# Kernel tuning notes

Hardware: AMD Instinct MI355X
Metric: run time of the kernel (lower is better)

Reference implementation:

```python
import jax, jax.numpy as jnp
import numpy as np
import math

DIM = 1024
THETA = 10000.0


def rope_cos_sin(seq_len, dim, dtype=jnp.float32):
    # freqs over pairs: 1/theta^(2i/dim), angles = t * freq
    inv = 1.0 / (THETA ** (jnp.arange(0, dim, 2, dtype=jnp.float32) / dim))  # [dim/2]
    t = jnp.arange(seq_len, dtype=jnp.float32)
    ang = jnp.outer(t, inv)  # [S, dim/2]
    return jnp.cos(ang).astype(dtype), jnp.sin(ang).astype(dtype)


def apply_rotary(x, cos, sin):
    # x: [B, S, D]; treat consecutive pairs as complex (xr + i*xi)
    B, S, D = x.shape
    xr = x[..., 0::2]  # [B, S, D/2]
    xi = x[..., 1::2]
    or_ = xr * cos - xi * sin
    oi_ = xr * sin + xi * cos
    # interleave back: (..., D/2, 2) -> (..., D)
    return jnp.stack([or_, oi_], axis=-1).reshape(B, S, D)


def setup_inputs() -> dict:
    key = jax.random.key(0)
    ks = jax.random.split(key, 5)
    B, S, D = 4, 2048, DIM
    x = jax.random.normal(ks[0], (B, S, D), dtype=jnp.float32)
    s = 1.0 / math.sqrt(D)
    wq = jax.random.normal(ks[1], (D, D), dtype=jnp.float32) * s
    wk = jax.random.normal(ks[2], (D, D), dtype=jnp.float32) * s
    wv = jax.random.normal(ks[3], (D, D), dtype=jnp.float32) * s
    wo = jax.random.normal(ks[4], (D, D), dtype=jnp.float32) * s
    return {"x": x, "wq": wq, "wk": wk, "wv": wv, "wo": wo}


def reference(x, wq, wk, wv, wo):
    B, S, D = x.shape
    xq = jnp.einsum('bsd,ed->bse', x, wq)  # Linear: x @ W^T
    xk = jnp.einsum('bsd,ed->bse', x, wk)
    xv = jnp.einsum('bsd,ed->bse', x, wv)
    cos, sin = rope_cos_sin(S, D, x.dtype)
    xq = apply_rotary(xq, cos, sin)
    xk = apply_rotary(xk, cos, sin)
    scores = jnp.einsum('bqd,bkd->bqk', xq, xk) / jnp.sqrt(jnp.asarray(D, x.dtype))
    attn = jax.nn.softmax(scores, axis=-1)  # no causal mask in original
    out = jnp.einsum('bqk,bkd->bqd', attn, xv)
    return jnp.einsum('bsd,ed->bse', out, wo)
```

## Files before the change

### kernel.cpp

```cpp
#include <hip/hip_runtime.h>
#include <math.h>

typedef __attribute__((ext_vector_type(8))) short short8;
typedef __attribute__((ext_vector_type(4))) float f32x4;
typedef unsigned short u16;

__device__ __forceinline__ float b2f(u16 u) {
    union { unsigned u; float f; } c; c.u = ((unsigned)u) << 16; return c.f;
}
__device__ __forceinline__ u16 f2b(float f) {
    unsigned u = __float_as_uint(f);
    u += 0x7fffu + ((u >> 16) & 1u);
    return (u16)(u >> 16);
}

__device__ __forceinline__ void gl_lds16(const u16* g, u16* l) {
    __builtin_amdgcn_global_load_lds(
        (const __attribute__((address_space(1))) void*)g,
        (__attribute__((address_space(3))) void*)l,
        16, 0, 0);
}

__device__ __forceinline__ void xcd_swz(int& bx, int& by) {
    const int nxy = gridDim.x * gridDim.y;
    const int l = blockIdx.x + gridDim.x * blockIdx.y;
    const int l2 = (l & 7) * (nxy >> 3) + (l >> 3);
    bx = l2 % gridDim.x;
    by = l2 / gridDim.x;
}

__global__ __launch_bounds__(256) void cvt_all(
    const float* __restrict__ x,
    const float* __restrict__ w0, const float* __restrict__ w1,
    const float* __restrict__ w2, const float* __restrict__ w3,
    u16* __restrict__ xb, u16* __restrict__ wb)
{
    const int b = blockIdx.x;
    const float* src; u16* dst; int i;
    if (b < 4096) {
        i = (b * 256 + threadIdx.x) * 8;
        src = x; dst = xb;
    } else {
        const int j = b - 4096;
        const int z = j >> 9;
        src = (z == 0) ? w0 : (z == 1) ? w1 : (z == 2) ? w2 : w3;
        i = ((j & 511) * 256 + threadIdx.x) * 8;
        dst = wb + (long)z * 1024 * 1024;
    }
    const float4 a = *(const float4*)&src[i];
    const float4 c = *(const float4*)&src[i + 4];
    short8 o;
    o[0] = (short)f2b(a.x); o[1] = (short)f2b(a.y);
    o[2] = (short)f2b(a.z); o[3] = (short)f2b(a.w);
    o[4] = (short)f2b(c.x); o[5] = (short)f2b(c.y);
    o[6] = (short)f2b(c.z); o[7] = (short)f2b(c.w);
    *(short8*)&dst[i] = o;
}

template<typename OT>
__device__ __forceinline__ void gemm_body(
    const u16* __restrict__ A, const u16* __restrict__ W, OT* __restrict__ C,
    int lda, int ldw, int ldc, int K, float scale, int bx, int by)
{
    __shared__ u16 lsA[2][128 * 32];
    __shared__ u16 lsB[2][128 * 32];

    const int m0 = by * 128;
    const int n0 = bx * 128;
    const int t = threadIdx.x;
    const int lane = t & 63;
    const int wave = t >> 6;
    const int wm = (wave & 1) * 64;
    const int wn = (wave >> 1) * 64;

    const int sr = t >> 2;
    const int scol = ((t & 3) ^ ((t >> 3) & 3)) * 8;

    const u16* pa0 = A + (long)(m0 + sr) * lda + scol;
    const u16* pa1 = pa0 + (long)64 * lda;
    const u16* pw0 = W + (long)(n0 + sr) * ldw + scol;
    const u16* pw1 = pw0 + (long)64 * ldw;

    f32x4 acc[4][4];
#pragma unroll
    for (int i = 0; i < 4; ++i)
#pragma unroll
        for (int j = 0; j < 4; ++j)
            acc[i][j] = (f32x4){0.f, 0.f, 0.f, 0.f};

    const int fr = lane & 15;
    const int fq = lane >> 4;
    const int swz = (fq ^ ((fr >> 1) & 3)) * 8;
    const int aoff = (wm + fr) * 32 + swz;
    const int boff = (wn + fr) * 32 + swz;

    gl_lds16(pa0, &lsA[0][t * 8]);        pa0 += 32;
    gl_lds16(pa1, &lsA[0][2048 + t * 8]); pa1 += 32;
    gl_lds16(pw0, &lsB[0][t * 8]);        pw0 += 32;
    gl_lds16(pw1, &lsB[0][2048 + t * 8]); pw1 += 32;

    const int nsteps = K >> 5;
    int par = 0;
    for (int s = 0; s < nsteps; ++s) {
        __syncthreads();
        if (s + 1 < nsteps) {
            const int np = par ^ 1;
            gl_lds16(pa0, &lsA[np][t * 8]);        pa0 += 32;
            gl_lds16(pa1, &lsA[np][2048 + t * 8]); pa1 += 32;
            gl_lds16(pw0, &lsB[np][t * 8]);        pw0 += 32;
            gl_lds16(pw1, &lsB[np][2048 + t * 8]); pw1 += 32;
        }

        short8 af[4], bf[4];
#pragma unroll
        for (int i = 0; i < 4; ++i)
            af[i] = *(const short8*)&lsA[par][aoff + i * 512];
#pragma unroll
        for (int j = 0; j < 4; ++j)
            bf[j] = *(const short8*)&lsB[par][boff + j * 512];
#pragma unroll
        for (int i = 0; i < 4; ++i)
#pragma unroll
            for (int j = 0; j < 4; ++j)
                acc[i][j] = __builtin_amdgcn_mfma_f32_16x16x32_bf16(af[i], bf[j], acc[i][j], 0, 0, 0);
        par ^= 1;
    }

#pragma unroll
    for (int i = 0; i < 4; ++i) {
#pragma unroll
        for (int j = 0; j < 4; ++j) {
            const int row0 = m0 + wm + i * 16 + fq * 4;
            const int col = n0 + wn + j * 16 + fr;
#pragma unroll
            for (int r = 0; r < 4; ++r) {
                const int row = row0 + r;
                const float val = acc[i][j][r] * scale;
                if (sizeof(OT) == 2) {
                    ((u16*)C)[(long)row * ldc + col] = f2b(val);
                } else {
                    ((float*)C)[(long)row * ldc + col] = val;
                }
            }
        }
    }
}

template<typename OT>
__global__ __launch_bounds__(256) void gemm_bt(
    const u16* __restrict__ A, const u16* __restrict__ W, OT* __restrict__ C,
    int lda, int ldw, int ldc, int K,
    long sA, long sW, long sC, float scale)
{
    int bx, by;
    xcd_swz(bx, by);
    const int bz = blockIdx.z;
    gemm_body<OT>(A + (long)bz * sA, W + (long)bz * sW, C + (long)bz * sC,
                  lda, ldw, ldc, K, scale, bx, by);
}

__global__ __launch_bounds__(256) void gemm_dual(
    const u16* __restrict__ A0, const u16* __restrict__ W0, u16* __restrict__ C0,
    int lda0, int ldw0, int ldc0, long sA0, long sW0, long sC0, float scale0,
    const u16* __restrict__ A1, const u16* __restrict__ W1, u16* __restrict__ C1,
    int lda1, int ldw1, int ldc1, long sA1, long sW1, long sC1, float scale1)
{
    const int z = blockIdx.z;
    if (z < 4) {
        int bx, by;
        xcd_swz(bx, by);
        gemm_body<u16>(A0 + (long)z * sA0, W0 + (long)z * sW0, C0 + (long)z * sC0,
                       lda0, ldw0, ldc0, 1024, scale0, bx, by);
    } else {
        if (blockIdx.y >= 8) return;
        const int b = z - 4;
        gemm_body<u16>(A1 + (long)b * sA1, W1 + (long)b * sW1, C1 + (long)b * sC1,
                       lda1, ldw1, ldc1, 1024, scale1, blockIdx.x, blockIdx.y);
    }
}

__global__ __launch_bounds__(256) void rope_kernel(u16* q, u16* k) {
    const int row = blockIdx.x;
    const int pos = row & 2047;
    u16* p = (blockIdx.y ? k : q) + (long)row * 1024;
#pragma unroll
    for (int it = 0; it < 2; ++it) {
        const int i = threadIdx.x + it * 256;
        const float e = (float)i * (1.0f / 512.0f);
        const float inv = powf(10000.0f, -e);
        const float ang = (float)pos * inv;
        float s, c;
        sincosf(ang, &s, &c);
        const float xr = b2f(p[2 * i]);
        const float xi = b2f(p[2 * i + 1]);
        p[2 * i]     = f2b(xr * c - xi * s);
        p[2 * i + 1] = f2b(xr * s + xi * c);
    }
}

__global__ __launch_bounds__(256) void softmax_kernel(const u16* __restrict__ S, u16* __restrict__ P) {
    const long row = blockIdx.x;
    const u16* src = S + row * 2048;
    u16* dst = P + row * 2048;
    const int t = threadIdx.x;
    const int lane = t & 63;
    const int wave = t >> 6;
    __shared__ float red[4];

    float v[8];
    const short8 raw = *(const short8*)&src[t * 8];
#pragma unroll
    for (int i = 0; i < 8; ++i) v[i] = b2f((u16)raw[i]);

    float m = v[0];
#pragma unroll
    for (int i = 1; i < 8; ++i) m = fmaxf(m, v[i]);
    for (int o = 32; o > 0; o >>= 1) m = fmaxf(m, __shfl_xor(m, o, 64));
    if (lane == 0) red[wave] = m;
    __syncthreads();
    m = fmaxf(fmaxf(red[0], red[1]), fmaxf(red[2], red[3]));
    __syncthreads();

    float sum = 0.f;
#pragma unroll
    for (int i = 0; i < 8; ++i) { v[i] = expf(v[i] - m); sum += v[i]; }
    for (int o = 32; o > 0; o >>= 1) sum += __shfl_xor(sum, o, 64);
    if (lane == 0) red[wave] = sum;
    __syncthreads();
    sum = red[0] + red[1] + red[2] + red[3];
    const float is = 1.0f / sum;

    short8 outv;
#pragma unroll
    for (int i = 0; i < 8; ++i) outv[i] = (short)f2b(v[i] * is);
    *(short8*)&dst[t * 8] = outv;
}

extern "C" void kernel_launch(void* const* d_in, const int* in_sizes, int n_in,
                              void* d_out, int out_size, void* d_ws, size_t ws_size,
                              hipStream_t stream)
{
    (void)in_sizes; (void)n_in; (void)out_size; (void)ws_size;
    const float* x  = (const float*)d_in[0];
    const float* wq = (const float*)d_in[1];
    const float* wk = (const float*)d_in[2];
    const float* wv = (const float*)d_in[3];
    const float* wo = (const float*)d_in[4];
    float* out = (float*)d_out;

    const long M1 = 1024 * 1024;
    u16* ws  = (u16*)d_ws;
    u16* xb  = ws;
    u16* wqb = xb + 8 * M1;
    u16* wob = wqb + 3 * M1;
    u16* q   = wqb + 4 * M1;
    u16* kk  = q + 8 * M1;
    u16* v   = kk + 8 * M1;
    u16* sc  = v + 8 * M1;
    u16* UT  = xb;

    const dim3 blk(256);

    cvt_all<<<dim3(6144), blk, 0, stream>>>(x, wq, wk, wv, wo, xb, wqb);

    gemm_bt<u16><<<dim3(8, 64, 3), blk, 0, stream>>>(xb, wqb, q,
        1024, 1024, 1024, 1024, 0, M1, 8 * M1, 1.0f);

    rope_kernel<<<dim3(8192, 2), blk, 0, stream>>>(q, kk);

    gemm_dual<<<dim3(16, 16, 8), blk, 0, stream>>>(
        q, kk, sc, 1024, 1024, 2048, 2 * M1, 2 * M1, 4 * M1, 0.03125f,
        wob, v, UT, 1024, 1024, 2048, 0, 2 * M1, 2 * M1, 1.0f);

    softmax_kernel<<<dim3(8192), blk, 0, stream>>>(sc, sc);

    gemm_bt<float><<<dim3(8, 16, 4), blk, 0, stream>>>(sc, UT, out,
        2048, 2048, 1024, 2048, 4 * M1, 2 * M1, 2 * M1, 1.0f);
}
```

Measured before the change: 317.8 us.

## Precompute RoPE tables and co-schedule Wo·V GEMM with the rotary pass

RoPE cos/sin values are precomputed into small factored tables (hi/lo position split combined by the angle-addition formula) inside the conversion kernel. This removes the per-element powf and sincosf work from the rotary pass. The rotary kernel now handles q and k together with vectorized 4-element accesses, and it also runs the Wo·V GEMM blocks, so that GEMM overlaps with the memory-bound rotary pass. The QK^T GEMM becomes a plain batched launch. The trade-off is extra table memory, and the angle-addition composition may shift rounding slightly.

Result: slower. 355.8 us (+12.0%).

```diff
diff --git a/kernel.cpp b/kernel.cpp
--- a/kernel.cpp
+++ b/kernel.cpp
@@ -33,9 +33,31 @@
     const float* __restrict__ x,
     const float* __restrict__ w0, const float* __restrict__ w1,
     const float* __restrict__ w2, const float* __restrict__ w3,
-    u16* __restrict__ xb, u16* __restrict__ wb)
+    u16* __restrict__ xb, u16* __restrict__ wb,
+    float* __restrict__ ct1, float* __restrict__ st1,
+    float* __restrict__ ct2, float* __restrict__ st2)
 {
     const int b = blockIdx.x;
+    if (b >= 6144) {
+        const int j = b - 6144;
+#pragma unroll
+        for (int it = 0; it < 2; ++it) {
+            const int f = threadIdx.x + it * 256;
+            const float inv = powf(10000.0f, -(float)f * (1.0f / 512.0f));
+            float sn, cs;
+            if (j < 32) {
+                sincosf((float)(j * 64) * inv, &sn, &cs);
+                ct1[f * 32 + j] = cs;
+                st1[f * 32 + j] = sn;
+            } else {
+                const int lo = j - 32;
+                sincosf((float)lo * inv, &sn, &cs);
+                ct2[f * 64 + lo] = cs;
+                st2[f * 64 + lo] = sn;
+            }
+        }
+        return;
+    }
     const float* src; u16* dst; int i;
     if (b < 4096) {
         i = (b * 256 + threadIdx.x) * 8;
@@ -159,43 +181,56 @@
                   lda, ldw, ldc, K, scale, bx, by);
 }
 
-__global__ __launch_bounds__(256) void gemm_dual(
-    const u16* __restrict__ A0, const u16* __restrict__ W0, u16* __restrict__ C0,
-    int lda0, int ldw0, int ldc0, long sA0, long sW0, long sC0, float scale0,
-    const u16* __restrict__ A1, const u16* __restrict__ W1, u16* __restrict__ C1,
-    int lda1, int ldw1, int ldc1, long sA1, long sW1, long sC1, float scale1)
-{
-    const int z = blockIdx.z;
-    if (z < 4) {
-        int bx, by;
-        xcd_swz(bx, by);
-        gemm_body<u16>(A0 + (long)z * sA0, W0 + (long)z * sW0, C0 + (long)z * sC0,
-                       lda0, ldw0, ldc0, 1024, scale0, bx, by);
-    } else {
-        if (blockIdx.y >= 8) return;
-        const int b = z - 4;
-        gemm_body<u16>(A1 + (long)b * sA1, W1 + (long)b * sW1, C1 + (long)b * sC1,
-                       lda1, ldw1, ldc1, 1024, scale1, blockIdx.x, blockIdx.y);
-    }
-}
-
-__global__ __launch_bounds__(256) void rope_kernel(u16* q, u16* k) {
-    const int row = blockIdx.x;
+__global__ __launch_bounds__(256) void rope_ut(
+    u16* __restrict__ q, u16* __restrict__ k,
+    const float* __restrict__ ct1, const float* __restrict__ st1,
+    const float* __restrict__ ct2, const float* __restrict__ st2,
+    const u16* __restrict__ wob, const u16* __restrict__ v, u16* __restrict__ UT)
+{
+    const long M1 = 1024 * 1024;
+    const int b = blockIdx.x;
+    if (b < 512) {
+        const int batch = b >> 7;
+        const int bx = b & 15;
+        const int by = (b >> 4) & 7;
+        gemm_body<u16>(wob, v + (long)batch * 2 * M1, UT + (long)batch * 2 * M1,
+                       1024, 1024, 2048, 1024, 1.0f, bx, by);
+        return;
+    }
+    const int row = b - 512;
     const int pos = row & 2047;
-    u16* p = (blockIdx.y ? k : q) + (long)row * 1024;
-#pragma unroll
-    for (int it = 0; it < 2; ++it) {
-        const int i = threadIdx.x + it * 256;
-        const float e = (float)i * (1.0f / 512.0f);
-        const float inv = powf(10000.0f, -e);
-        const float ang = (float)pos * inv;
-        float s, c;
-        sincosf(ang, &s, &c);
-        const float xr = b2f(p[2 * i]);
-        const float xi = b2f(p[2 * i + 1]);
-        p[2 * i]     = f2b(xr * c - xi * s);
-        p[2 * i + 1] = f2b(xr * s + xi * c);
-    }
+    const int hi = pos >> 6;
+    const int lo = pos & 63;
+    const int t = threadIdx.x;
+    const int f0 = 2 * t;
+
+    const float c1a = ct1[f0 * 32 + hi],       s1a = st1[f0 * 32 + hi];
+    const float c2a = ct2[f0 * 64 + lo],       s2a = st2[f0 * 64 + lo];
+    const float c1b = ct1[(f0 + 1) * 32 + hi], s1b = st1[(f0 + 1) * 32 + hi];
+    const float c2b = ct2[(f0 + 1) * 64 + lo], s2b = st2[(f0 + 1) * 64 + lo];
+    const float ca = c1a * c2a - s1a * s2a, sa = s1a * c2a + c1a * s2a;
+    const float cb = c1b * c2b - s1b * s2b, sb = s1b * c2b + c1b * s2b;
+
+    u16* pq = q + (long)row * 1024 + 4 * t;
+    u16* pk = k + (long)row * 1024 + 4 * t;
+
+    ushort4 vq = *(ushort4*)pq;
+    {
+        const float xr0 = b2f(vq.x), xi0 = b2f(vq.y);
+        const float xr1 = b2f(vq.z), xi1 = b2f(vq.w);
+        vq.x = f2b(xr0 * ca - xi0 * sa); vq.y = f2b(xr0 * sa + xi0 * ca);
+        vq.z = f2b(xr1 * cb - xi1 * sb); vq.w = f2b(xr1 * sb + xi1 * cb);
+    }
+    *(ushort4*)pq = vq;
+
+    ushort4 vk = *(ushort4*)pk;
+    {
+        const float xr0 = b2f(vk.x), xi0 = b2f(vk.y);
+        const float xr1 = b2f(vk.z), xi1 = b2f(vk.w);
+        vk.x = f2b(xr0 * ca - xi0 * sa); vk.y = f2b(xr0 * sa + xi0 * ca);
+        vk.z = f2b(xr1 * cb - xi1 * sb); vk.w = f2b(xr1 * sb + xi1 * cb);
+    }
+    *(ushort4*)pk = vk;
 }
 
 __global__ __launch_bounds__(256) void softmax_kernel(const u16* __restrict__ S, u16* __restrict__ P) {
@@ -258,19 +293,24 @@
     u16* v   = kk + 8 * M1;
     u16* sc  = v + 8 * M1;
     u16* UT  = xb;
+    float* ct1 = (float*)(sc + 16 * M1);
+    float* st1 = ct1 + 512 * 32;
+    float* ct2 = st1 + 512 * 32;
+    float* st2 = ct2 + 512 * 64;
 
     const dim3 blk(256);
 
-    cvt_all<<<dim3(6144), blk, 0, stream>>>(x, wq, wk, wv, wo, xb, wqb);
+    cvt_all<<<dim3(6240), blk, 0, stream>>>(x, wq, wk, wv, wo, xb, wqb,
+                                            ct1, st1, ct2, st2);
 
     gemm_bt<u16><<<dim3(8, 64, 3), blk, 0, stream>>>(xb, wqb, q,
         1024, 1024, 1024, 1024, 0, M1, 8 * M1, 1.0f);
 
-    rope_kernel<<<dim3(8192, 2), blk, 0, stream>>>(q, kk);
-
-    gemm_dual<<<dim3(16, 16, 8), blk, 0, stream>>>(
-        q, kk, sc, 1024, 1024, 2048, 2 * M1, 2 * M1, 4 * M1, 0.03125f,
-        wob, v, UT, 1024, 1024, 2048, 0, 2 * M1, 2 * M1, 1.0f);
+    rope_ut<<<dim3(512 + 8192), blk, 0, stream>>>(q, kk, ct1, st1, ct2, st2,
+                                                  wob, v, UT);
+
+    gemm_bt<u16><<<dim3(16, 16, 4), blk, 0, stream>>>(q, kk, sc,
+        1024, 1024, 2048, 1024, 2 * M1, 2 * M1, 4 * M1, 0.03125f);
 
     softmax_kernel<<<dim3(8192), blk, 0, stream>>>(sc, sc);
 
```
